# Optimization experiments

Hardware: AMD Instinct MI355X
Metric: run time of the kernel (lower is better)

## Reference

```python
import jax, jax.numpy as jnp
import numpy as np

B, n, A = 64, 1024, 32          # graphs, nodes/graph, actions/graph
N = B * n
EH = 2048                        # undirected edges per graph
HID, H = 128, 4
C = HID // H
NF, EF, AD, NI, L = 1, 1, 7, 4, 3
NEG_SLOPE = 0.2


def setup_inputs() -> dict:
    ks = jax.random.split(jax.random.key(0), 16)
    x = jax.random.normal(ks[0], (N, NF), jnp.float32)
    s = jax.random.randint(ks[1], (B, EH), 0, n)
    d = jax.random.randint(ks[2], (B, EH), 0, n)
    off = (jnp.arange(B) * n)[:, None]
    s = (s + off).reshape(-1)
    d = (d + off).reshape(-1)
    # bidirectional edges (unrooted trees): both i->j and j->i
    edge_index = jnp.stack([jnp.concatenate([s, d]), jnp.concatenate([d, s])]).astype(jnp.int32)
    E = edge_index.shape[1]
    edge_attr = jax.random.uniform(ks[3], (E, EF), jnp.float32)
    idx = jax.random.randint(ks[4], (B, A, NI), 0, n).astype(jnp.float32)
    meta = jax.random.normal(ks[5], (B, A, AD - NI), jnp.float32)
    action_tensor = jnp.concatenate([idx, meta], axis=-1)
    batch_idx = jnp.repeat(jnp.arange(B, dtype=jnp.int32), n)
    batch_ptr = jnp.arange(B + 1, dtype=jnp.int32) * n

    def lin(k, i, o):
        return jax.random.normal(k, (i, o), jnp.float32) / np.float32(np.sqrt(i))

    inp = dict(x=x, edge_attr=edge_attr, action_tensor=action_tensor,
               edge_index=edge_index, batch_idx=batch_idx, batch_ptr=batch_ptr)
    inp["Wn"] = lin(ks[6], NF, HID); inp["bn"] = jnp.zeros((HID,), jnp.float32)
    kl = jax.random.split(ks[7], 4 * L)
    inp["gWl"] = jnp.stack([lin(kl[i], HID, HID) for i in range(L)])
    inp["gWr"] = jnp.stack([lin(kl[L + i], HID, HID) for i in range(L)])
    inp["gWe"] = jnp.stack([lin(kl[2 * L + i], EF, HID) for i in range(L)])
    inp["gatt"] = jnp.stack([jax.random.normal(kl[3 * L + i], (H, C), jnp.float32) * 0.1 for i in range(L)])
    inp["gbl"] = jnp.zeros((L, HID), jnp.float32)
    inp["gbr"] = jnp.zeros((L, HID), jnp.float32)
    inp["gb"] = jnp.zeros((L, HID), jnp.float32)
    mlp_in = NI * HID + (AD - NI)
    inp["aW1"] = lin(ks[8], mlp_in, HID); inp["ab1"] = jnp.zeros((HID,), jnp.float32)
    inp["aW2"] = lin(ks[9], HID, HID); inp["ab2"] = jnp.zeros((HID,), jnp.float32)
    inp["qW1"] = lin(ks[10], 4 * HID, HID); inp["qb1"] = jnp.zeros((HID,), jnp.float32)
    inp["qW2"] = lin(ks[11], HID, HID); inp["qb2"] = jnp.zeros((HID,), jnp.float32)
    inp["qW3"] = lin(ks[12], HID, 1); inp["qb3"] = jnp.zeros((1,), jnp.float32)
    return inp


def _gatv2(h, src, dst, ea, Wl, bl, Wr, br, We, att, b):
    # PyG GATv2Conv: e_ij = att . leaky_relu(lin_l(x_j) + lin_r(x_i) + lin_edge(e_ij))
    Nn = h.shape[0]
    xl = (h @ Wl + bl).reshape(Nn, H, C)   # source transform
    xr = (h @ Wr + br).reshape(Nn, H, C)   # target transform
    ee = (ea @ We).reshape(-1, H, C)       # edge transform (no bias in PyG)
    e = jax.nn.leaky_relu(xl[src] + xr[dst] + ee, NEG_SLOPE)   # [E,H,C]
    logits = jnp.einsum('ehc,hc->eh', e, att)
    m = jax.ops.segment_max(logits, dst, num_segments=Nn)       # stable softmax per target node
    ex = jnp.exp(logits - m[dst])
    alpha = ex / jax.ops.segment_sum(ex, dst, num_segments=Nn)[dst]
    msg = (xl[src] * alpha[:, :, None]).reshape(-1, HID)
    return jax.ops.segment_sum(msg, dst, num_segments=Nn) + b


def reference(x, edge_attr, action_tensor, Wn, bn, gWl, gbl, gWr, gbr, gWe, gatt, gb,
              aW1, ab1, aW2, ab2, qW1, qb1, qW2, qb2, qW3, qb3,
              edge_index, batch_idx, batch_ptr):
    Nn = x.shape[0]
    nb = batch_ptr.shape[0] - 1
    # GATv2Conv default add_self_loops=True, fill_value='mean' for edge_attr
    loops = jnp.arange(Nn, dtype=edge_index.dtype)
    src = jnp.concatenate([edge_index[0], loops])
    dst = jnp.concatenate([edge_index[1], loops])
    ea = jnp.concatenate([edge_attr, jnp.broadcast_to(edge_attr.mean(0), (Nn, edge_attr.shape[1]))], 0)
    h = jax.nn.relu(x @ Wn + bn)
    for l in range(L):
        h = jax.nn.relu(_gatv2(h, src, dst, ea, gWl[l], gbl[l], gWr[l], gbr[l], gWe[l], gatt[l], gb[l])) + h
    # sum / mean / max pooling per graph
    sums = jax.ops.segment_sum(h, batch_idx, num_segments=nb)
    cnt = jax.ops.segment_sum(jnp.ones((Nn, 1), h.dtype), batch_idx, num_segments=nb)
    means = sums / cnt
    maxs = jax.ops.segment_max(h, batch_idx, num_segments=nb)
    tree_emb = jnp.concatenate([sums, means, maxs], -1)          # [B, 3*HID]
    # action encoding: gather node embeddings at action node indices (shifted by batch_ptr)
    ni = action_tensor[..., :NI].astype(jnp.int32) + batch_ptr[:-1][:, None, None]
    g = h[ni].reshape(nb, action_tensor.shape[1], NI * HID)
    ai = jnp.concatenate([g, action_tensor[..., NI:]], -1)
    ae = jax.nn.relu(jax.nn.relu(ai @ aW1 + ab1) @ aW2 + ab2)    # [B, A, HID]
    comb = jnp.concatenate([jnp.broadcast_to(tree_emb[:, None, :], (nb, ae.shape[1], 3 * HID)), ae], -1)
    q = jax.nn.relu(comb @ qW1 + qb1)
    q = jax.nn.relu(q @ qW2 + qb2)
    return (q @ qW3 + qb3).squeeze(-1)                            # [B, A]
```

## Files before the change

### kernel.cpp

```cpp
#include <hip/hip_runtime.h>
#include <hip/hip_bf16.h>

#define NNODES 65536
#define NGRAPH 64
#define NPG 1024
#define NACT 32
#define HID 128
#define NHEAD 4
#define CPH 32

typedef __attribute__((ext_vector_type(8))) short bf16x8;
typedef __attribute__((ext_vector_type(4))) float f32x4;

__device__ __forceinline__ void load8(float* dst, const float* src) {
    float4 q0 = ((const float4*)src)[0];
    float4 q1 = ((const float4*)src)[1];
    dst[0]=q0.x; dst[1]=q0.y; dst[2]=q0.z; dst[3]=q0.w;
    dst[4]=q1.x; dst[5]=q1.y; dst[6]=q1.z; dst[7]=q1.w;
}

__device__ __forceinline__ void load8bf(float* dst, const unsigned short* src) {
    uint4 q = *(const uint4*)src;
    unsigned int u0 = q.x, u1 = q.y, u2 = q.z, u3 = q.w;
    dst[0] = __uint_as_float(u0 << 16); dst[1] = __uint_as_float(u0 & 0xffff0000u);
    dst[2] = __uint_as_float(u1 << 16); dst[3] = __uint_as_float(u1 & 0xffff0000u);
    dst[4] = __uint_as_float(u2 << 16); dst[5] = __uint_as_float(u2 & 0xffff0000u);
    dst[6] = __uint_as_float(u3 << 16); dst[7] = __uint_as_float(u3 & 0xffff0000u);
}

__device__ __forceinline__ unsigned short f2bf(float f) {
    unsigned int u = __float_as_uint(f);
    u = (u + 0x7fffu + ((u >> 16) & 1u)) >> 16;
    return (unsigned short)u;
}


__global__ void hist_mean_k(const int* __restrict__ ei, const float* __restrict__ ea,
                            int* __restrict__ deg, float* __restrict__ meansum, int E0) {
    __shared__ float s[256];
    int t = threadIdx.x;
    int e = blockIdx.x * 256 + t;
    float v = 0.f;
    if (e < E0) {
        atomicAdd(&deg[ei[E0 + e]], 1);
        v = ea[e];
    }
    s[t] = v; __syncthreads();
    for (int off = 128; off > 0; off >>= 1) { if (t < off) s[t] += s[t+off]; __syncthreads(); }
    if (t == 0) atomicAdd(meansum, s[0]);
}

__global__ void scan_bsum_k(const int* __restrict__ deg, int* __restrict__ bsum) {
    __shared__ int s[256];
    int t = threadIdx.x;
    s[t] = deg[blockIdx.x * 256 + t]; __syncthreads();
    for (int off = 128; off > 0; off >>= 1) { if (t < off) s[t] += s[t+off]; __syncthreads(); }
    if (t == 0) bsum[blockIdx.x] = s[0];
}

__global__ void scan_boff_k(const int* __restrict__ bsum, int* __restrict__ boff) {
    __shared__ int s[256];
    int t = threadIdx.x;
    s[t] = bsum[t]; __syncthreads();
    for (int off = 1; off < 256; off <<= 1) {
        int v = (t >= off) ? s[t-off] : 0; __syncthreads();
        s[t] += v; __syncthreads();
    }
    boff[t] = s[t] - bsum[t];
}

__global__ void scan_rowptr_k(const int* __restrict__ deg, const int* __restrict__ boff,
                              int* __restrict__ rowptr, int N, int E0) {
    __shared__ int s[256];
    int t = threadIdx.x;
    int i = blockIdx.x * 256 + t;
    int d = deg[i];
    s[t] = d; __syncthreads();
    for (int off = 1; off < 256; off <<= 1) {
        int v = (t >= off) ? s[t-off] : 0; __syncthreads();
        s[t] += v; __syncthreads();
    }
    rowptr[i] = boff[blockIdx.x] + s[t] - d;
    if (i == N - 1) rowptr[N] = E0;
}

__global__ void scatter_k(const int* __restrict__ ei, const float* __restrict__ ea,
                          const int* __restrict__ rowptr, int* __restrict__ cursor,
                          int* __restrict__ csr_src, float* __restrict__ csr_ea, int E0) {
    int e = blockIdx.x * 256 + threadIdx.x;
    if (e >= E0) return;
    int s = ei[e], d = ei[E0 + e];
    int pos = atomicAdd(&cursor[d], 1);
    int slot = rowptr[d] + pos;
    csr_src[slot] = s;
    csr_ea[slot]  = ea[e];
}

__global__ void prep_k(const float* __restrict__ gWl, const float* __restrict__ gWr,
                       unsigned short* __restrict__ wtl, unsigned short* __restrict__ wtr,
                       const float* __restrict__ aW1, const float* __restrict__ aW2,
                       const float* __restrict__ qW1, const float* __restrict__ qW2,
                       unsigned short* __restrict__ wA1t, unsigned short* __restrict__ wA2t,
                       unsigned short* __restrict__ wQ1t, unsigned short* __restrict__ wQ2t) {
    int bid = blockIdx.x, t = threadIdx.x;
    if (bid < 192) {
        int idx = bid * 256 + t;
        int l = idx >> 14, rem = idx & 16383;
        int n = rem >> 7, k = rem & 127;
        int src = l*16384 + k*128 + n;
        wtl[idx] = f2bf(gWl[src]);
        wtr[idx] = f2bf(gWr[src]);
    } else {
        int n = bid - 192;
        for (int k = t; k < 544; k += 256)
            wA1t[n*544 + k] = (k < 515) ? f2bf(aW1[(size_t)k*128 + n]) : (unsigned short)0;
        if (t < 128) {
            wA2t[n*128 + t] = f2bf(aW2[(size_t)t*128 + n]);
            wQ1t[n*128 + t] = f2bf(qW1[(size_t)(384 + t)*128 + n]);
            wQ2t[n*128 + t] = f2bf(qW2[(size_t)t*128 + n]);
        }
    }
}

__global__ void node_init_k(const float* __restrict__ x, const float* __restrict__ Wn,
                            const float* __restrict__ bn, float* __restrict__ h,
                            unsigned short* __restrict__ hb) {
    int idx = blockIdx.x * 256 + threadIdx.x;
    int i = idx >> 7, f = idx & 127;
    float v = x[i] * Wn[f] + bn[f];
    v = v > 0.f ? v : 0.f;
    h[idx] = v;
    hb[idx] = f2bf(v);
}

__global__ __launch_bounds__(256) void gemm_lr_mfma_k(
    const unsigned short* __restrict__ hb,
    const unsigned short* __restrict__ wtl, const unsigned short* __restrict__ wtr,
    const float* __restrict__ bl, const float* __restrict__ br,
    unsigned short* __restrict__ xlb, float* __restrict__ xr) {
    int wave = threadIdx.x >> 6;
    int lane = threadIdx.x & 63;
    int lr = lane & 15;
    int lq = lane >> 4;
    int r0 = blockIdx.x * 128 + wave * 32;

    const short* hs = (const short*)hb;
    bf16x8 a[2][4];
#pragma unroll
    for (int rt = 0; rt < 2; ++rt)
#pragma unroll
        for (int kf = 0; kf < 4; ++kf)
            a[rt][kf] = *(const bf16x8*)(hs + (size_t)(r0 + rt*16 + lr)*HID + kf*32 + lq*8);

    const short* ws[2]   = {(const short*)wtl, (const short*)wtr};
    const float* bias[2] = {bl, br};

#pragma unroll
    for (int m = 0; m < 2; ++m) {
        const short* W = ws[m];
        f32x4 acc[2][8];
#pragma unroll
        for (int rt = 0; rt < 2; ++rt)
#pragma unroll
            for (int ct = 0; ct < 8; ++ct) acc[rt][ct] = (f32x4){0.f,0.f,0.f,0.f};

        bf16x8 b[4], nb[4];
#pragma unroll
        for (int kf = 0; kf < 4; ++kf)
            b[kf] = *(const bf16x8*)(W + (size_t)(lr)*HID + kf*32 + lq*8);
#pragma unroll
        for (int ct = 0; ct < 8; ++ct) {
            if (ct < 7) {
#pragma unroll
                for (int kf = 0; kf < 4; ++kf)
                    nb[kf] = *(const bf16x8*)(W + (size_t)((ct+1)*16 + lr)*HID + kf*32 + lq*8);
            }
#pragma unroll
            for (int rt = 0; rt < 2; ++rt)
#pragma unroll
                for (int kf = 0; kf < 4; ++kf)
                    acc[rt][ct] = __builtin_amdgcn_mfma_f32_16x16x32_bf16(a[rt][kf], b[kf], acc[rt][ct], 0, 0, 0);
#pragma unroll
            for (int kf = 0; kf < 4; ++kf) b[kf] = nb[kf];
        }
#pragma unroll
        for (int ct = 0; ct < 8; ++ct) {
            float bv = bias[m][ct*16 + lr];
#pragma unroll
            for (int rt = 0; rt < 2; ++rt)
#pragma unroll
                for (int rg = 0; rg < 4; ++rg) {
                    int row = r0 + rt*16 + lq*4 + rg;
                    float val = acc[rt][ct][rg] + bv;
                    if (m == 0) xlb[(size_t)row*HID + ct*16 + lr] = f2bf(val);
                    else        xr [(size_t)row*HID + ct*16 + lr] = val;
                }
        }
    }
}

__global__ __launch_bounds__(256, 8) void gat_edge_k(
    const unsigned short* __restrict__ xlb, const float* __restrict__ xr,
    float* __restrict__ h, unsigned short* __restrict__ hb,
    const int* __restrict__ rowptr, const int* __restrict__ csr_src,
    const float* __restrict__ csr_ea,
    const float* __restrict__ We, const float* __restrict__ att,
    const float* __restrict__ gb, const float* __restrict__ meansum, float inv_e0) {
    __shared__ int   s_src[2048];
    __shared__ float s_ea[2048];
    int xcd  = blockIdx.x & 7;
    int slot = blockIdx.x >> 3;
    int g    = xcd * 8 + (slot >> 6);
    int j    = slot & 63;
    int t    = threadIdx.x;
    int vb   = g * NPG + j * 16;
    int v    = vb + (t >> 4);
    int li   = t & 15;
    int base = li * 8;
    float mea = meansum[0] * inv_e0;

    int span0 = rowptr[vb];
    int cnt   = rowptr[vb + 16] - span0;
    for (int i = t; i < cnt && i < 2048; i += 256) {
        s_src[i] = csr_src[span0 + i];
        s_ea[i]  = csr_ea[span0 + i];
    }
    __syncthreads();

    float xrv[8], attv[8], wev[8];
    load8(xrv, xr + (size_t)v*HID + base);
    load8(attv, att + base);
    load8(wev, We + base);

    float acc[8], xn[8];
    load8bf(xn, xlb + (size_t)v*HID + base);
    float m;
    {
        float lg = 0.f;
#pragma unroll
        for (int c = 0; c < 8; ++c) {
            float e = xn[c] + xrv[c] + mea * wev[c];
            e = fmaxf(e, 0.2f * e);
            lg = fmaf(attv[c], e, lg);
        }
        lg += __shfl_xor(lg, 1, 64);
        lg += __shfl_xor(lg, 2, 64);
        m = lg;
#pragma unroll
        for (int c = 0; c < 8; ++c) acc[c] = xn[c];
    }
    float den = 1.f;

    int s0 = rowptr[v] - span0, s1 = rowptr[v+1] - span0;
    if (s0 < s1) {
        float an = s_ea[s0];
        load8bf(xn, xlb + (size_t)s_src[s0]*HID + base);
        for (int i = s0; i < s1; ++i) {
            int i2 = (i + 1 < s1) ? (i + 1) : s0;
            int   sidx2 = s_src[i2];
            float a2    = s_ea[i2];
            float x2[8];
            load8bf(x2, xlb + (size_t)sidx2*HID + base);

            float lg = 0.f;
#pragma unroll
            for (int c = 0; c < 8; ++c) {
                float e = xn[c] + xrv[c] + an * wev[c];
                e = fmaxf(e, 0.2f * e);
                lg = fmaf(attv[c], e, lg);
            }
            lg += __shfl_xor(lg, 1, 64);
            lg += __shfl_xor(lg, 2, 64);

            float mn  = fmaxf(m, lg);
            float sc  = __expf(m - mn);
            float wgt = __expf(lg - mn);
            den = den * sc + wgt;
#pragma unroll
            for (int c = 0; c < 8; ++c) acc[c] = acc[c] * sc + wgt * xn[c];
            m = mn;
            an = a2;
#pragma unroll
            for (int c = 0; c < 8; ++c) xn[c] = x2[c];
        }
    }

    float inv = 1.f / den;
    size_t o = (size_t)v*HID + base;
    float hold[8], gbv[8];
    load8(hold, h + o);
    load8(gbv, gb + base);
    float nh[8];
#pragma unroll
    for (int c = 0; c < 8; ++c) {
        float val = acc[c] * inv + gbv[c];
        val = val > 0.f ? val : 0.f;
        nh[c] = val + hold[c];
    }
    float4* hp = (float4*)(h + o);
    hp[0] = make_float4(nh[0], nh[1], nh[2], nh[3]);
    hp[1] = make_float4(nh[4], nh[5], nh[6], nh[7]);
    unsigned int* hbp = (unsigned int*)(hb + o);
#pragma unroll
    for (int q = 0; q < 4; ++q)
        hbp[q] = (unsigned int)f2bf(nh[2*q]) | ((unsigned int)f2bf(nh[2*q+1]) << 16);
}

__global__ __launch_bounds__(256) void pool_k(const float* __restrict__ h,
                                              float* __restrict__ tree_sum,
                                              float* __restrict__ tree_max) {
    int b = blockIdx.x >> 3, chunk = blockIdx.x & 7;
    int t = threadIdx.x, col = t & 127, half = t >> 7;
    const float* hb_ = h + ((size_t)b * NPG + chunk * 128 + half * 64) * HID;
    float s = 0.f, mx = 0.f;
    for (int i = 0; i < 64; ++i) {
        float v = hb_[(size_t)i*HID + col];
        s += v; mx = fmaxf(mx, v);
    }
    __shared__ float sb[2][128], mb[2][128];
    sb[half][col] = s; mb[half][col] = mx;
    __syncthreads();
    if (half == 0) {
        s  = sb[0][col] + sb[1][col];
        mx = fmaxf(mb[0][col], mb[1][col]);
        atomicAdd(&tree_sum[b*128 + col], s);
        atomicMax((int*)&tree_max[b*128 + col], __float_as_int(mx));
    }
}

#define SA1 552
#define SAC 136
__global__ __launch_bounds__(256) void action_q_k(
    const unsigned short* __restrict__ hb, const float* __restrict__ action,
    const int* __restrict__ batch_ptr,
    const float* __restrict__ tree_sum, const float* __restrict__ tree_max,
    const unsigned short* __restrict__ wA1t, const float* __restrict__ ab1,
    const unsigned short* __restrict__ wA2t, const float* __restrict__ ab2,
    const float* __restrict__ qW1, const unsigned short* __restrict__ wQ1t,
    const float* __restrict__ qb1,
    const unsigned short* __restrict__ wQ2t, const float* __restrict__ qb2,
    const float* __restrict__ qW3, const float* __restrict__ qb3,
    float* __restrict__ out) {
    int b = blockIdx.x;
    int t = threadIdx.x;
    int w  = t >> 6;
    int lane = t & 63;
    int lr = lane & 15;
    int lq = lane >> 4;

    __shared__ unsigned short aib[32 * SA1];
    __shared__ unsigned short z1s[32 * SAC];
    __shared__ unsigned short aes[32 * SAC];
    __shared__ unsigned short q1s[32 * SAC];
    __shared__ float q2f[32 * 132];
    __shared__ float tqA[128], tqB[128];
    __shared__ float psum[32][8];

    int ptr = batch_ptr[b];

    {
        int p = t >> 1, half = t & 1;
        int a = p >> 2, j = p & 3;
        const float* actp = action + (size_t)(b * NACT + a) * 7;
        int ni = (int)actp[j] + ptr;
        const uint4* src = (const uint4*)(hb + (size_t)ni * HID) + half * 8;
        uint4* dst = (uint4*)((char*)aib + ((size_t)a * SA1 + j * 128 + half * 64) * 2);
#pragma unroll
        for (int q = 0; q < 8; ++q) dst[q] = src[q];
        if (t < 32) {
            const float* ap = action + (size_t)(b * NACT + t) * 7;
            aib[t * SA1 + 512] = f2bf(ap[4]);
            aib[t * SA1 + 513] = f2bf(ap[5]);
            aib[t * SA1 + 514] = f2bf(ap[6]);
            for (int i = 3; i < 40; ++i) aib[t * SA1 + 512 + i] = 0;
        }
    }

    {
        if (t < 128) {
            int col = t;
            float acc = 0.f;
#pragma unroll 4
            for (int k = 0; k < 128; ++k) {
                float sv = tree_sum[b * 128 + k];
                acc = fmaf(sv, qW1[(size_t)k * 128 + col], acc);
                acc = fmaf(sv * (1.f / 1024.f), qW1[(size_t)(128 + k) * 128 + col], acc);
            }
            tqA[col] = acc;
        } else {
            int col = t - 128;
            float acc = 0.f;
#pragma unroll 4
            for (int k = 0; k < 128; ++k) {
                float mv = tree_max[b * 128 + k];
                acc = fmaf(mv, qW1[(size_t)(256 + k) * 128 + col], acc);
            }
            tqB[col] = acc;
        }
    }
    __syncthreads();

    f32x4 acc[2][2];
    const unsigned short* srcA;
    int strideA, K;

    srcA = aib; strideA = SA1; K = 544;
#pragma unroll
    for (int rt = 0; rt < 2; ++rt)
#pragma unroll
        for (int ci = 0; ci < 2; ++ci) acc[rt][ci] = (f32x4){0.f, 0.f, 0.f, 0.f};
    for (int ks = 0; ks < K; ks += 32) {
        bf16x8 a0 = *(const bf16x8*)(srcA + (0 * 16 + lr) * strideA + ks + lq * 8);
        bf16x8 a1 = *(const bf16x8*)(srcA + (1 * 16 + lr) * strideA + ks + lq * 8);
        bf16x8 b0 = *(const bf16x8*)(wA1t + (size_t)((2 * w + 0) * 16 + lr) * K + ks + lq * 8);
        bf16x8 b1 = *(const bf16x8*)(wA1t + (size_t)((2 * w + 1) * 16 + lr) * K + ks + lq * 8);
        acc[0][0] = __builtin_amdgcn_mfma_f32_16x16x32_bf16(a0, b0, acc[0][0], 0, 0, 0);
        acc[0][1] = __builtin_amdgcn_mfma_f32_16x16x32_bf16(a0, b1, acc[0][1], 0, 0, 0);
        acc[1][0] = __builtin_amdgcn_mfma_f32_16x16x32_bf16(a1, b0, acc[1][0], 0, 0, 0);
        acc[1][1] = __builtin_amdgcn_mfma_f32_16x16x32_bf16(a1, b1, acc[1][1], 0, 0, 0);
    }
#pragma unroll
    for (int ci = 0; ci < 2; ++ci) {
        int col = (2 * w + ci) * 16 + lr;
        float bv = ab1[col];
#pragma unroll
        for (int rt = 0; rt < 2; ++rt)
#pragma unroll
            for (int rg = 0; rg < 4; ++rg) {
                int row = rt * 16 + lq * 4 + rg;
                z1s[row * SAC + col] = f2bf(fmaxf(acc[rt][ci][rg] + bv, 0.f));
            }
    }
    __syncthreads();

    srcA = z1s; strideA = SAC; K = 128;
#pragma unroll
    for (int rt = 0; rt < 2; ++rt)
#pragma unroll
        for (int ci = 0; ci < 2; ++ci) acc[rt][ci] = (f32x4){0.f, 0.f, 0.f, 0.f};
#pragma unroll
    for (int ks = 0; ks < 128; ks += 32) {
        bf16x8 a0 = *(const bf16x8*)(srcA + (0 * 16 + lr) * strideA + ks + lq * 8);
        bf16x8 a1 = *(const bf16x8*)(srcA + (1 * 16 + lr) * strideA + ks + lq * 8);
        bf16x8 b0 = *(const bf16x8*)(wA2t + (size_t)((2 * w + 0) * 16 + lr) * K + ks + lq * 8);
        bf16x8 b1 = *(const bf16x8*)(wA2t + (size_t)((2 * w + 1) * 16 + lr) * K + ks + lq * 8);
        acc[0][0] = __builtin_amdgcn_mfma_f32_16x16x32_bf16(a0, b0, acc[0][0], 0, 0, 0);
        acc[0][1] = __builtin_amdgcn_mfma_f32_16x16x32_bf16(a0, b1, acc[0][1], 0, 0, 0);
        acc[1][0] = __builtin_amdgcn_mfma_f32_16x16x32_bf16(a1, b0, acc[1][0], 0, 0, 0);
        acc[1][1] = __builtin_amdgcn_mfma_f32_16x16x32_bf16(a1, b1, acc[1][1], 0, 0, 0);
    }
#pragma unroll
    for (int ci = 0; ci < 2; ++ci) {
        int col = (2 * w + ci) * 16 + lr;
        float bv = ab2[col];
#pragma unroll
        for (int rt = 0; rt < 2; ++rt)
#pragma unroll
            for (int rg = 0; rg < 4; ++rg) {
                int row = rt * 16 + lq * 4 + rg;
                aes[row * SAC + col] = f2bf(fmaxf(acc[rt][ci][rg] + bv, 0.f));
            }
    }
    __syncthreads();

    srcA = aes; strideA = SAC; K = 128;
#pragma unroll
    for (int rt = 0; rt < 2; ++rt)
#pragma unroll
        for (int ci = 0; ci < 2; ++ci) acc[rt][ci] = (f32x4){0.f, 0.f, 0.f, 0.f};
#pragma unroll
    for (int ks = 0; ks < 128; ks += 32) {
        bf16x8 a0 = *(const bf16x8*)(srcA + (0 * 16 + lr) * strideA + ks + lq * 8);
        bf16x8 a1 = *(const bf16x8*)(srcA + (1 * 16 + lr) * strideA + ks + lq * 8);
        bf16x8 b0 = *(const bf16x8*)(wQ1t + (size_t)((2 * w + 0) * 16 + lr) * K + ks + lq * 8);
        bf16x8 b1 = *(const bf16x8*)(wQ1t + (size_t)((2 * w + 1) * 16 + lr) * K + ks + lq * 8);
        acc[0][0] = __builtin_amdgcn_mfma_f32_16x16x32_bf16(a0, b0, acc[0][0], 0, 0, 0);
        acc[0][1] = __builtin_amdgcn_mfma_f32_16x16x32_bf16(a0, b1, acc[0][1], 0, 0, 0);
        acc[1][0] = __builtin_amdgcn_mfma_f32_16x16x32_bf16(a1, b0, acc[1][0], 0, 0, 0);
        acc[1][1] = __builtin_amdgcn_mfma_f32_16x16x32_bf16(a1, b1, acc[1][1], 0, 0, 0);
    }
#pragma unroll
    for (int ci = 0; ci < 2; ++ci) {
        int col = (2 * w + ci) * 16 + lr;
        float bv = qb1[col] + tqA[col] + tqB[col];
#pragma unroll
        for (int rt = 0; rt < 2; ++rt)
#pragma unroll
            for (int rg = 0; rg < 4; ++rg) {
                int row = rt * 16 + lq * 4 + rg;
                q1s[row * SAC + col] = f2bf(fmaxf(acc[rt][ci][rg] + bv, 0.f));
            }
    }
    __syncthreads();

    srcA = q1s; strideA = SAC; K = 128;
#pragma unroll
    for (int rt = 0; rt < 2; ++rt)
#pragma unroll
        for (int ci = 0; ci < 2; ++ci) acc[rt][ci] = (f32x4){0.f, 0.f, 0.f, 0.f};
#pragma unroll
    for (int ks = 0; ks < 128; ks += 32) {
        bf16x8 a0 = *(const bf16x8*)(srcA + (0 * 16 + lr) * strideA + ks + lq * 8);
        bf16x8 a1 = *(const bf16x8*)(srcA + (1 * 16 + lr) * strideA + ks + lq * 8);
        bf16x8 b0 = *(const bf16x8*)(wQ2t + (size_t)((2 * w + 0) * 16 + lr) * K + ks + lq * 8);
        bf16x8 b1 = *(const bf16x8*)(wQ2t + (size_t)((2 * w + 1) * 16 + lr) * K + ks + lq * 8);
        acc[0][0] = __builtin_amdgcn_mfma_f32_16x16x32_bf16(a0, b0, acc[0][0], 0, 0, 0);
        acc[0][1] = __builtin_amdgcn_mfma_f32_16x16x32_bf16(a0, b1, acc[0][1], 0, 0, 0);
        acc[1][0] = __builtin_amdgcn_mfma_f32_16x16x32_bf16(a1, b0, acc[1][0], 0, 0, 0);
        acc[1][1] = __builtin_amdgcn_mfma_f32_16x16x32_bf16(a1, b1, acc[1][1], 0, 0, 0);
    }
#pragma unroll
    for (int ci = 0; ci < 2; ++ci) {
        int col = (2 * w + ci) * 16 + lr;
        float bv = qb2[col];
#pragma unroll
        for (int rt = 0; rt < 2; ++rt)
#pragma unroll
            for (int rg = 0; rg < 4; ++rg) {
                int row = rt * 16 + lq * 4 + rg;
                q2f[row * 132 + col] = fmaxf(acc[rt][ci][rg] + bv, 0.f);
            }
    }
    __syncthreads();

    {
        int a = t >> 3, seg = t & 7;
        float s = 0.f;
#pragma unroll
        for (int k = 0; k < 16; ++k)
            s = fmaf(q2f[a * 132 + seg * 16 + k], qW3[seg * 16 + k], s);
        psum[a][seg] = s;
    }
    __syncthreads();
    if (t < 32) {
        float s = qb3[0];
#pragma unroll
        for (int i = 0; i < 8; ++i) s += psum[t][i];
        out[(size_t)b * NACT + t] = s;
    }
}

extern "C" void kernel_launch(void* const* d_in, const int* in_sizes, int n_in,
                              void* d_out, int out_size, void* d_ws, size_t ws_size,
                              hipStream_t stream) {
    const float* x         = (const float*)d_in[0];
    const float* edge_attr = (const float*)d_in[1];
    const float* action    = (const float*)d_in[2];
    const int*   edge_idx  = (const int*)d_in[3];
    const int*   batch_ptr = (const int*)d_in[5];
    const float* Wn  = (const float*)d_in[6];
    const float* bn  = (const float*)d_in[7];
    const float* gWl = (const float*)d_in[8];
    const float* gWr = (const float*)d_in[9];
    const float* gWe = (const float*)d_in[10];
    const float* gatt= (const float*)d_in[11];
    const float* gbl = (const float*)d_in[12];
    const float* gbr = (const float*)d_in[13];
    const float* gb  = (const float*)d_in[14];
    const float* aW1 = (const float*)d_in[15];
    const float* ab1 = (const float*)d_in[16];
    const float* aW2 = (const float*)d_in[17];
    const float* ab2 = (const float*)d_in[18];
    const float* qW1 = (const float*)d_in[19];
    const float* qb1 = (const float*)d_in[20];
    const float* qW2 = (const float*)d_in[21];
    const float* qb2 = (const float*)d_in[22];
    const float* qW3 = (const float*)d_in[23];
    const float* qb3 = (const float*)d_in[24];
    float* out = (float*)d_out;

    const int E0 = in_sizes[1];
    const int N  = NNODES;

    char* w = (char*)d_ws;
    auto alloc = [&](size_t bytes) { void* p = (void*)w; w += (bytes + 255) & ~(size_t)255; return p; };
    float* h        = (float*)alloc((size_t)N * HID * 4);
    unsigned short* hb  = (unsigned short*)alloc((size_t)N * HID * 2);
    unsigned short* xlb = (unsigned short*)alloc((size_t)N * HID * 2);
    float* xr       = (float*)alloc((size_t)N * HID * 4);
    int*   rowptr   = (int*)alloc((size_t)(N + 1) * 4);
    int*   deg      = (int*)alloc((size_t)N * 4);
    int*   cursor   = (int*)alloc((size_t)N * 4);
    float* meansum  = (float*)alloc(256);
    float* tree_sum = (float*)alloc((size_t)NGRAPH * 128 * 4);
    float* tree_max = (float*)alloc((size_t)NGRAPH * 128 * 4);
    size_t zero_span = (size_t)((char*)(tree_max + NGRAPH * 128) - (char*)deg);
    int*   bsum     = (int*)alloc(256 * 4);
    int*   boff     = (int*)alloc(256 * 4);
    int*   csr_src  = (int*)alloc((size_t)E0 * 4);
    float* csr_ea   = (float*)alloc((size_t)E0 * 4);
    unsigned short* wtl = (unsigned short*)alloc((size_t)3*128*128*2);
    unsigned short* wtr = (unsigned short*)alloc((size_t)3*128*128*2);
    unsigned short* wA1t = (unsigned short*)alloc((size_t)128*544*2);
    unsigned short* wA2t = (unsigned short*)alloc((size_t)128*128*2);
    unsigned short* wQ1t = (unsigned short*)alloc((size_t)128*128*2);
    unsigned short* wQ2t = (unsigned short*)alloc((size_t)128*128*2);

    hipMemsetAsync(deg, 0, zero_span, stream);

    int eb = (E0 + 255) / 256;
    hist_mean_k<<<eb, 256, 0, stream>>>(edge_idx, edge_attr, deg, meansum, E0);
    scan_bsum_k<<<N/256, 256, 0, stream>>>(deg, bsum);
    scan_boff_k<<<1, 256, 0, stream>>>(bsum, boff);
    scan_rowptr_k<<<N/256, 256, 0, stream>>>(deg, boff, rowptr, N, E0);
    scatter_k<<<eb, 256, 0, stream>>>(edge_idx, edge_attr, rowptr, cursor, csr_src, csr_ea, E0);

    prep_k<<<320, 256, 0, stream>>>(gWl, gWr, wtl, wtr,
                                    aW1, aW2, qW1, qW2, wA1t, wA2t, wQ1t, wQ2t);
    node_init_k<<<(N * HID) / 256, 256, 0, stream>>>(x, Wn, bn, h, hb);

    float inv_e0 = 1.0f / (float)E0;
    for (int l = 0; l < 3; ++l) {
        gemm_lr_mfma_k<<<N / 128, 256, 0, stream>>>(
            hb, wtl + (size_t)l*128*128, wtr + (size_t)l*128*128,
            gbl + l*HID, gbr + l*HID, xlb, xr);
        gat_edge_k<<<N / 16, 256, 0, stream>>>(
            xlb, xr, h, hb, rowptr, csr_src, csr_ea,
            gWe + l*HID, gatt + l*NHEAD*CPH, gb + l*HID, meansum, inv_e0);
    }

    pool_k<<<NGRAPH * 8, 256, 0, stream>>>(h, tree_sum, tree_max);

    action_q_k<<<NGRAPH, 256, 0, stream>>>(
        hb, action, batch_ptr, tree_sum, tree_max,
        wA1t, ab1, wA2t, ab2, qW1, wQ1t, qb1, wQ2t, qb2, qW3, qb3, out);
}
```

Baseline: 347.1 us.

## Replace CSR scan with fixed-slot adjacency and fuse setup, node init and pooling

```diff
diff --git a/kernel.cpp b/kernel.cpp
--- a/kernel.cpp
+++ b/kernel.cpp
@@ -6,8 +6,7 @@
 #define NPG 1024
 #define NACT 32
 #define HID 128
-#define NHEAD 4
-#define CPH 32
+#define DEGS 64
 
 typedef __attribute__((ext_vector_type(8))) short bf16x8;
 typedef __attribute__((ext_vector_type(4))) float f32x4;
@@ -34,84 +33,38 @@
     return (unsigned short)u;
 }
 
-
-__global__ void hist_mean_k(const int* __restrict__ ei, const float* __restrict__ ea,
-                            int* __restrict__ deg, float* __restrict__ meansum, int E0) {
-    __shared__ float s[256];
-    int t = threadIdx.x;
-    int e = blockIdx.x * 256 + t;
-    float v = 0.f;
-    if (e < E0) {
-        atomicAdd(&deg[ei[E0 + e]], 1);
-        v = ea[e];
-    }
-    s[t] = v; __syncthreads();
-    for (int off = 128; off > 0; off >>= 1) { if (t < off) s[t] += s[t+off]; __syncthreads(); }
-    if (t == 0) atomicAdd(meansum, s[0]);
-}
-
-__global__ void scan_bsum_k(const int* __restrict__ deg, int* __restrict__ bsum) {
-    __shared__ int s[256];
-    int t = threadIdx.x;
-    s[t] = deg[blockIdx.x * 256 + t]; __syncthreads();
-    for (int off = 128; off > 0; off >>= 1) { if (t < off) s[t] += s[t+off]; __syncthreads(); }
-    if (t == 0) bsum[blockIdx.x] = s[0];
-}
-
-__global__ void scan_boff_k(const int* __restrict__ bsum, int* __restrict__ boff) {
-    __shared__ int s[256];
-    int t = threadIdx.x;
-    s[t] = bsum[t]; __syncthreads();
-    for (int off = 1; off < 256; off <<= 1) {
-        int v = (t >= off) ? s[t-off] : 0; __syncthreads();
-        s[t] += v; __syncthreads();
-    }
-    boff[t] = s[t] - bsum[t];
-}
-
-__global__ void scan_rowptr_k(const int* __restrict__ deg, const int* __restrict__ boff,
-                              int* __restrict__ rowptr, int N, int E0) {
-    __shared__ int s[256];
-    int t = threadIdx.x;
-    int i = blockIdx.x * 256 + t;
-    int d = deg[i];
-    s[t] = d; __syncthreads();
-    for (int off = 1; off < 256; off <<= 1) {
-        int v = (t >= off) ? s[t-off] : 0; __syncthreads();
-        s[t] += v; __syncthreads();
-    }
-    rowptr[i] = boff[blockIdx.x] + s[t] - d;
-    if (i == N - 1) rowptr[N] = E0;
-}
-
-__global__ void scatter_k(const int* __restrict__ ei, const float* __restrict__ ea,
-                          const int* __restrict__ rowptr, int* __restrict__ cursor,
-                          int* __restrict__ csr_src, float* __restrict__ csr_ea, int E0) {
-    int e = blockIdx.x * 256 + threadIdx.x;
-    if (e >= E0) return;
-    int s = ei[e], d = ei[E0 + e];
-    int pos = atomicAdd(&cursor[d], 1);
-    int slot = rowptr[d] + pos;
-    csr_src[slot] = s;
-    csr_ea[slot]  = ea[e];
-}
-
-__global__ void prep_k(const float* __restrict__ gWl, const float* __restrict__ gWr,
-                       unsigned short* __restrict__ wtl, unsigned short* __restrict__ wtr,
-                       const float* __restrict__ aW1, const float* __restrict__ aW2,
-                       const float* __restrict__ qW1, const float* __restrict__ qW2,
-                       unsigned short* __restrict__ wA1t, unsigned short* __restrict__ wA2t,
-                       unsigned short* __restrict__ wQ1t, unsigned short* __restrict__ wQ2t) {
+__global__ void setup_k(const int* __restrict__ ei, const float* __restrict__ ea,
+                        int* __restrict__ cursor, float* __restrict__ meansum,
+                        int2* __restrict__ csr, int E0, int nsb,
+                        const float* __restrict__ gWl, const float* __restrict__ gWr,
+                        unsigned short* __restrict__ wtl, unsigned short* __restrict__ wtr,
+                        const float* __restrict__ aW1, const float* __restrict__ aW2,
+                        const float* __restrict__ qW1, const float* __restrict__ qW2,
+                        unsigned short* __restrict__ wA1t, unsigned short* __restrict__ wA2t,
+                        unsigned short* __restrict__ wQ1t, unsigned short* __restrict__ wQ2t) {
     int bid = blockIdx.x, t = threadIdx.x;
-    if (bid < 192) {
-        int idx = bid * 256 + t;
+    if (bid < nsb) {
+        __shared__ float s[256];
+        int e = bid * 256 + t;
+        float v = 0.f;
+        if (e < E0) {
+            int sn = ei[e], d = ei[E0 + e];
+            int pos = atomicAdd(&cursor[d], 1);
+            csr[(size_t)d * DEGS + pos] = make_int2(sn, __float_as_int(ea[e]));
+            v = ea[e];
+        }
+        s[t] = v; __syncthreads();
+        for (int off = 128; off > 0; off >>= 1) { if (t < off) s[t] += s[t+off]; __syncthreads(); }
+        if (t == 0) atomicAdd(meansum, s[0]);
+    } else if (bid < nsb + 192) {
+        int idx = (bid - nsb) * 256 + t;
         int l = idx >> 14, rem = idx & 16383;
         int n = rem >> 7, k = rem & 127;
         int src = l*16384 + k*128 + n;
         wtl[idx] = f2bf(gWl[src]);
         wtr[idx] = f2bf(gWr[src]);
     } else {
-        int n = bid - 192;
+        int n = bid - nsb - 192;
         for (int k = t; k < 544; k += 256)
             wA1t[n*544 + k] = (k < 515) ? f2bf(aW1[(size_t)k*128 + n]) : (unsigned short)0;
         if (t < 128) {
@@ -122,38 +75,46 @@
     }
 }
 
-__global__ void node_init_k(const float* __restrict__ x, const float* __restrict__ Wn,
-                            const float* __restrict__ bn, float* __restrict__ h,
-                            unsigned short* __restrict__ hb) {
-    int idx = blockIdx.x * 256 + threadIdx.x;
-    int i = idx >> 7, f = idx & 127;
-    float v = x[i] * Wn[f] + bn[f];
-    v = v > 0.f ? v : 0.f;
-    h[idx] = v;
-    hb[idx] = f2bf(v);
-}
-
 __global__ __launch_bounds__(256) void gemm_lr_mfma_k(
-    const unsigned short* __restrict__ hb,
+    const unsigned short* __restrict__ hb, const float* __restrict__ x,
+    const float* __restrict__ Wn, const float* __restrict__ bn, int l0,
     const unsigned short* __restrict__ wtl, const unsigned short* __restrict__ wtr,
     const float* __restrict__ bl, const float* __restrict__ br,
-    unsigned short* __restrict__ xlb, float* __restrict__ xr) {
+    unsigned short* __restrict__ xlb, unsigned short* __restrict__ xrb) {
     int wave = threadIdx.x >> 6;
     int lane = threadIdx.x & 63;
     int lr = lane & 15;
     int lq = lane >> 4;
     int r0 = blockIdx.x * 128 + wave * 32;
 
-    const short* hs = (const short*)hb;
     bf16x8 a[2][4];
-#pragma unroll
-    for (int rt = 0; rt < 2; ++rt)
-#pragma unroll
-        for (int kf = 0; kf < 4; ++kf)
-            a[rt][kf] = *(const bf16x8*)(hs + (size_t)(r0 + rt*16 + lr)*HID + kf*32 + lq*8);
+    if (l0) {
+        float xv0 = x[r0 + lr], xv1 = x[r0 + 16 + lr];
+#pragma unroll
+        for (int kf = 0; kf < 4; ++kf) {
+            float wn[8], bv[8];
+            load8(wn, Wn + kf*32 + lq*8);
+            load8(bv, bn + kf*32 + lq*8);
+            union { bf16x8 v; unsigned short u[8]; } p0, p1;
+#pragma unroll
+            for (int j = 0; j < 8; ++j) {
+                p0.u[j] = f2bf(fmaxf(fmaf(xv0, wn[j], bv[j]), 0.f));
+                p1.u[j] = f2bf(fmaxf(fmaf(xv1, wn[j], bv[j]), 0.f));
+            }
+            a[0][kf] = p0.v; a[1][kf] = p1.v;
+        }
+    } else {
+        const short* hs = (const short*)hb;
+#pragma unroll
+        for (int rt = 0; rt < 2; ++rt)
+#pragma unroll
+            for (int kf = 0; kf < 4; ++kf)
+                a[rt][kf] = *(const bf16x8*)(hs + (size_t)(r0 + rt*16 + lr)*HID + kf*32 + lq*8);
+    }
 
     const short* ws[2]   = {(const short*)wtl, (const short*)wtr};
     const float* bias[2] = {bl, br};
+    unsigned short* outp[2] = {xlb, xrb};
 
 #pragma unroll
     for (int m = 0; m < 2; ++m) {
@@ -191,44 +152,35 @@
 #pragma unroll
                 for (int rg = 0; rg < 4; ++rg) {
                     int row = r0 + rt*16 + lq*4 + rg;
-                    float val = acc[rt][ct][rg] + bv;
-                    if (m == 0) xlb[(size_t)row*HID + ct*16 + lr] = f2bf(val);
-                    else        xr [(size_t)row*HID + ct*16 + lr] = val;
+                    outp[m][(size_t)row*HID + ct*16 + lr] = f2bf(acc[rt][ct][rg] + bv);
                 }
         }
     }
 }
 
 __global__ __launch_bounds__(256, 8) void gat_edge_k(
-    const unsigned short* __restrict__ xlb, const float* __restrict__ xr,
+    const unsigned short* __restrict__ xlb, const unsigned short* __restrict__ xrb,
     float* __restrict__ h, unsigned short* __restrict__ hb,
-    const int* __restrict__ rowptr, const int* __restrict__ csr_src,
-    const float* __restrict__ csr_ea,
+    const int* __restrict__ deg, const int2* __restrict__ csr,
     const float* __restrict__ We, const float* __restrict__ att,
-    const float* __restrict__ gb, const float* __restrict__ meansum, float inv_e0) {
-    __shared__ int   s_src[2048];
-    __shared__ float s_ea[2048];
+    const float* __restrict__ gb, const float* __restrict__ meansum, float inv_e0,
+    const float* __restrict__ x, const float* __restrict__ Wn, const float* __restrict__ bn,
+    int l0, int do_pool, float* __restrict__ tree_sum, float* __restrict__ tree_max) {
+    __shared__ float ps[16][132];
+    __shared__ float pm[16][132];
     int xcd  = blockIdx.x & 7;
     int slot = blockIdx.x >> 3;
     int g    = xcd * 8 + (slot >> 6);
     int j    = slot & 63;
     int t    = threadIdx.x;
-    int vb   = g * NPG + j * 16;
-    int v    = vb + (t >> 4);
+    int nd   = t >> 4;
+    int v    = g * NPG + j * 16 + nd;
     int li   = t & 15;
     int base = li * 8;
     float mea = meansum[0] * inv_e0;
 
-    int span0 = rowptr[vb];
-    int cnt   = rowptr[vb + 16] - span0;
-    for (int i = t; i < cnt && i < 2048; i += 256) {
-        s_src[i] = csr_src[span0 + i];
-        s_ea[i]  = csr_ea[span0 + i];
-    }
-    __syncthreads();
-
     float xrv[8], attv[8], wev[8];
-    load8(xrv, xr + (size_t)v*HID + base);
+    load8bf(xrv, xrb + (size_t)v*HID + base);
     load8(attv, att + base);
     load8(wev, We + base);
 
@@ -251,16 +203,17 @@
     }
     float den = 1.f;
 
-    int s0 = rowptr[v] - span0, s1 = rowptr[v+1] - span0;
-    if (s0 < s1) {
-        float an = s_ea[s0];
-        load8bf(xn, xlb + (size_t)s_src[s0]*HID + base);
-        for (int i = s0; i < s1; ++i) {
-            int i2 = (i + 1 < s1) ? (i + 1) : s0;
-            int   sidx2 = s_src[i2];
-            float a2    = s_ea[i2];
+    int dg = deg[v];
+    if (dg > 0) {
+        const int2* cp = csr + (size_t)v * DEGS;
+        int2 ec = cp[0];
+        int2 en = cp[dg > 1 ? 1 : 0];
+        load8bf(xn, xlb + (size_t)ec.x*HID + base);
+        for (int i = 0; i < dg; ++i) {
+            int2 e3 = cp[(i + 2 < dg) ? i + 2 : dg - 1];
             float x2[8];
-            load8bf(x2, xlb + (size_t)sidx2*HID + base);
+            load8bf(x2, xlb + (size_t)en.x*HID + base);
+            float an = __int_as_float(ec.y);
 
             float lg = 0.f;
 #pragma unroll
@@ -279,7 +232,7 @@
 #pragma unroll
             for (int c = 0; c < 8; ++c) acc[c] = acc[c] * sc + wgt * xn[c];
             m = mn;
-            an = a2;
+            ec = en; en = e3;
 #pragma unroll
             for (int c = 0; c < 8; ++c) xn[c] = x2[c];
         }
@@ -288,7 +241,16 @@
     float inv = 1.f / den;
     size_t o = (size_t)v*HID + base;
     float hold[8], gbv[8];
-    load8(hold, h + o);
+    if (l0) {
+        float xv = x[v];
+        float wn[8], bv[8];
+        load8(wn, Wn + base);
+        load8(bv, bn + base);
+#pragma unroll
+        for (int c = 0; c < 8; ++c) hold[c] = fmaxf(fmaf(xv, wn[c], bv[c]), 0.f);
+    } else {
+        load8(hold, h + o);
+    }
     load8(gbv, gb + base);
     float nh[8];
 #pragma unroll
@@ -304,27 +266,23 @@
 #pragma unroll
     for (int q = 0; q < 4; ++q)
         hbp[q] = (unsigned int)f2bf(nh[2*q]) | ((unsigned int)f2bf(nh[2*q+1]) << 16);
-}
-
-__global__ __launch_bounds__(256) void pool_k(const float* __restrict__ h,
-                                              float* __restrict__ tree_sum,
-                                              float* __restrict__ tree_max) {
-    int b = blockIdx.x >> 3, chunk = blockIdx.x & 7;
-    int t = threadIdx.x, col = t & 127, half = t >> 7;
-    const float* hb_ = h + ((size_t)b * NPG + chunk * 128 + half * 64) * HID;
-    float s = 0.f, mx = 0.f;
-    for (int i = 0; i < 64; ++i) {
-        float v = hb_[(size_t)i*HID + col];
-        s += v; mx = fmaxf(mx, v);
-    }
-    __shared__ float sb[2][128], mb[2][128];
-    sb[half][col] = s; mb[half][col] = mx;
-    __syncthreads();
-    if (half == 0) {
-        s  = sb[0][col] + sb[1][col];
-        mx = fmaxf(mb[0][col], mb[1][col]);
-        atomicAdd(&tree_sum[b*128 + col], s);
-        atomicMax((int*)&tree_max[b*128 + col], __float_as_int(mx));
+
+    if (do_pool) {
+#pragma unroll
+        for (int c = 0; c < 8; ++c) { ps[nd][base + c] = nh[c]; pm[nd][base + c] = nh[c]; }
+        __syncthreads();
+        if (t < 128) {
+            float s = 0.f;
+#pragma unroll
+            for (int n = 0; n < 16; ++n) s += ps[n][t];
+            atomicAdd(&tree_sum[g*128 + t], s);
+        } else {
+            int col = t - 128;
+            float mx = 0.f;
+#pragma unroll
+            for (int n = 0; n < 16; ++n) mx = fmaxf(mx, pm[n][col]);
+            atomicMax((int*)&tree_max[g*128 + col], __float_as_int(mx));
+        }
     }
 }
 
@@ -577,18 +535,13 @@
     float* h        = (float*)alloc((size_t)N * HID * 4);
     unsigned short* hb  = (unsigned short*)alloc((size_t)N * HID * 2);
     unsigned short* xlb = (unsigned short*)alloc((size_t)N * HID * 2);
-    float* xr       = (float*)alloc((size_t)N * HID * 4);
-    int*   rowptr   = (int*)alloc((size_t)(N + 1) * 4);
-    int*   deg      = (int*)alloc((size_t)N * 4);
+    unsigned short* xrb = (unsigned short*)alloc((size_t)N * HID * 2);
+    int2*  csr      = (int2*)alloc((size_t)N * DEGS * 8);
     int*   cursor   = (int*)alloc((size_t)N * 4);
     float* meansum  = (float*)alloc(256);
     float* tree_sum = (float*)alloc((size_t)NGRAPH * 128 * 4);
     float* tree_max = (float*)alloc((size_t)NGRAPH * 128 * 4);
-    size_t zero_span = (size_t)((char*)(tree_max + NGRAPH * 128) - (char*)deg);
-    int*   bsum     = (int*)alloc(256 * 4);
-    int*   boff     = (int*)alloc(256 * 4);
-    int*   csr_src  = (int*)alloc((size_t)E0 * 4);
-    float* csr_ea   = (float*)alloc((size_t)E0 * 4);
+    size_t zero_span = (size_t)((char*)(tree_max + NGRAPH * 128) - (char*)cursor);
     unsigned short* wtl = (unsigned short*)alloc((size_t)3*128*128*2);
     unsigned short* wtr = (unsigned short*)alloc((size_t)3*128*128*2);
     unsigned short* wA1t = (unsigned short*)alloc((size_t)128*544*2);
@@ -596,30 +549,24 @@
     unsigned short* wQ1t = (unsigned short*)alloc((size_t)128*128*2);
     unsigned short* wQ2t = (unsigned short*)alloc((size_t)128*128*2);
 
-    hipMemsetAsync(deg, 0, zero_span, stream);
-
-    int eb = (E0 + 255) / 256;
-    hist_mean_k<<<eb, 256, 0, stream>>>(edge_idx, edge_attr, deg, meansum, E0);
-    scan_bsum_k<<<N/256, 256, 0, stream>>>(deg, bsum);
-    scan_boff_k<<<1, 256, 0, stream>>>(bsum, boff);
-    scan_rowptr_k<<<N/256, 256, 0, stream>>>(deg, boff, rowptr, N, E0);
-    scatter_k<<<eb, 256, 0, stream>>>(edge_idx, edge_attr, rowptr, cursor, csr_src, csr_ea, E0);
-
-    prep_k<<<320, 256, 0, stream>>>(gWl, gWr, wtl, wtr,
-                                    aW1, aW2, qW1, qW2, wA1t, wA2t, wQ1t, wQ2t);
-    node_init_k<<<(N * HID) / 256, 256, 0, stream>>>(x, Wn, bn, h, hb);
+    hipMemsetAsync(cursor, 0, zero_span, stream);
+
+    int nsb = (E0 + 255) / 256;
+    setup_k<<<nsb + 320, 256, 0, stream>>>(edge_idx, edge_attr, cursor, meansum, csr, E0, nsb,
+                                           gWl, gWr, wtl, wtr,
+                                           aW1, aW2, qW1, qW2, wA1t, wA2t, wQ1t, wQ2t);
 
     float inv_e0 = 1.0f / (float)E0;
     for (int l = 0; l < 3; ++l) {
         gemm_lr_mfma_k<<<N / 128, 256, 0, stream>>>(
-            hb, wtl + (size_t)l*128*128, wtr + (size_t)l*128*128,
-            gbl + l*HID, gbr + l*HID, xlb, xr);
+            hb, x, Wn, bn, (l == 0) ? 1 : 0,
+            wtl + (size_t)l*128*128, wtr + (size_t)l*128*128,
+            gbl + l*HID, gbr + l*HID, xlb, xrb);
         gat_edge_k<<<N / 16, 256, 0, stream>>>(
-            xlb, xr, h, hb, rowptr, csr_src, csr_ea,
-            gWe + l*HID, gatt + l*NHEAD*CPH, gb + l*HID, meansum, inv_e0);
-    }
-
-    pool_k<<<NGRAPH * 8, 256, 0, stream>>>(h, tree_sum, tree_max);
+            xlb, xrb, h, hb, cursor, csr,
+            gWe + l*HID, gatt + l*128, gb + l*HID, meansum, inv_e0,
+            x, Wn, bn, (l == 0) ? 1 : 0, (l == 2) ? 1 : 0, tree_sum, tree_max);
+    }
 
     action_q_k<<<NGRAPH, 256, 0, stream>>>(
         hb, action, batch_ptr, tree_sum, tree_max,
```

Measured after the change: 312.4 us. 1.11x faster.
